# Performance work log

Measured on AMD Instinct MI355X. Metric: run time of the kernel, lower is better.

The kernel has to match this reference:

```python
import jax, jax.numpy as jnp
import numpy as np

NUM_CLS = 80
TOPK = 100
CONF_THRESH = 0.05
NMS_THRESH = 0.5
NKS_ALPHA = 0.6
INPUT_SIZE = (512, 512)  # (H, W)
STRIDES = (4, 8, 16, 32)
BATCH = 8


def _make_pixel_location():
    H, W = INPUT_SIZE
    locs = []
    for s in STRIDES:
        hs, ws = H // s, W // s
        ys, xs = np.meshgrid(np.arange(hs), np.arange(ws), indexing='ij')
        x = xs * s + s / 2.0
        y = ys * s + s / 2.0
        locs.append(np.stack([x, y, x, y], -1).reshape(-1, 4))
    return np.concatenate(locs, 0).astype(np.float32)  # [HW, 4]


def setup_inputs() -> dict:
    key = jax.random.key(0)
    pix = jnp.asarray(_make_pixel_location())
    HW = pix.shape[0]
    pred_head = jax.random.normal(key, (BATCH, HW, NUM_CLS + 5), dtype=jnp.float32)
    return {"pred_head": pred_head, "pixel_location": pix}


def _nms_single(boxes, scores, cls, valid):
    """Greedy per-class NMS on fixed-size TOPK candidates. Returns keep mask in original order."""
    N = scores.shape[0]
    order = jnp.argsort(-jnp.where(valid, scores, -jnp.inf))
    b = boxes[order]
    v = valid[order]
    c = cls[order]
    x1, y1, x2, y2 = b[:, 0], b[:, 1], b[:, 2], b[:, 3]
    areas = (x2 - x1) * (y2 - y1)
    xx1 = jnp.maximum(x1[:, None], x1[None, :])
    yy1 = jnp.maximum(y1[:, None], y1[None, :])
    xx2 = jnp.minimum(x2[:, None], x2[None, :])
    yy2 = jnp.minimum(y2[:, None], y2[None, :])
    w = jnp.maximum(1e-28, xx2 - xx1)
    h = jnp.maximum(1e-28, yy2 - yy1)
    inter = w * h
    ovr = inter / (areas[:, None] + areas[None, :] - inter)
    # original NMS is per-class: cross-class pairs never suppress
    ovr = jnp.where(c[:, None] == c[None, :], ovr, 0.0)
    idx = jnp.arange(N)

    def body(i, state):
        keep, sup = state
        ki = v[i] & jnp.logical_not(sup[i])
        keep = keep.at[i].set(ki)
        sup = sup | (ki & (ovr[i] > NMS_THRESH) & (idx > i))
        return (keep, sup)

    keep_sorted, _ = jax.lax.fori_loop(0, N, body, (jnp.zeros(N, bool), jnp.zeros(N, bool)))
    return jnp.zeros(N, bool).at[order].set(keep_sorted)


def reference(pred_head, pixel_location):
    B, HW, _ = pred_head.shape
    cls_pred = jax.nn.sigmoid(pred_head[:, :, :NUM_CLS])               # [B, HW, C]
    loc_w = jnp.array([[-1.0, -1.0, 1.0, 1.0]], dtype=pred_head.dtype)
    loc_pred = jax.nn.relu(pred_head[:, :, NUM_CLS:-1]) * loc_w + pixel_location[None]  # [B, HW, 4]
    nks = jax.nn.sigmoid(pred_head[:, :, -1:])
    nks = 1.0 / (1.0 + jnp.exp(-2.0 * nks + 1.0))
    cls_pred = jnp.power(cls_pred, (2.0 - nks) * NKS_ALPHA + 1e-14)

    def pool3x3(x):
        # torch F.max_pool2d on 3D [B,HW,C] pools 3x3 over the (HW, C) plane
        return jax.lax.reduce_window(x, -jnp.inf, jax.lax.max, (1, 3, 3), (1, 1, 1), 'SAME')

    def step(cmap, i):
        # original re-suppresses the shared heatmap on every batch iteration
        hmax = pool3x3(cmap)
        cmap = cmap * (hmax == cmap).astype(cmap.dtype)
        flat = jnp.transpose(cmap[i], (1, 0)).reshape(-1)  # class-major [C*HW], matches permute(1,0).view(-1)
        s, ind = jax.lax.top_k(flat, TOPK)
        return cmap, (s, ind)

    _, (topk_scores, topk_inds) = jax.lax.scan(step, cls_pred, jnp.arange(B))  # [B, TOPK]
    topk_cls = (topk_inds // HW).astype(jnp.int32)
    topk_hw = topk_inds % HW
    boxes = jnp.take_along_axis(loc_pred, topk_hw[:, :, None], axis=1)  # [B, TOPK, 4]
    valid = topk_scores > CONF_THRESH
    keep = jax.vmap(_nms_single)(boxes, topk_scores, topk_cls, valid)   # [B, TOPK] bool
    scale = jnp.array([INPUT_SIZE[1], INPUT_SIZE[0], INPUT_SIZE[1], INPUT_SIZE[0]], dtype=boxes.dtype)
    bboxes = jnp.clip(boxes / scale, 0.0, 1.0)
    return bboxes, topk_scores, topk_cls, keep
```

## Files before the change

### kernel.cpp

```cpp
#include <hip/hip_runtime.h>
#include <math.h>

#define BATCH   8
#define HW      21760
#define NCLS    80
#define NCH     85
#define TOPK    100
#define ABUF    128
#define CBUF    512
#define XTH     2.40f
#define STH     0x3F700000u
#define LTH     (-0.09315f)
#define RPB     128
#define TILES   170
#define F4PB    2720
#define SLOTP   128
#define NSLOT   (TILES * SLOTP)
#define NF4S    (NSLOT / 4)
#define SORTN   256
#define FBIN    256
#define FSH     12

#define LOG2E 1.44269504088896340736f
__device__ __forceinline__ float xsig(float x) { return 1.0f / (1.0f + expf(-x)); }
__device__ __forceinline__ float exact_score(const float* __restrict__ row, int c) {
    float p  = xsig(row[c]);
    float s1 = xsig(row[NCH - 1]);
    float n2 = 1.0f / (1.0f + expf(1.0f - 2.0f * s1));
    float e  = (2.0f - n2) * 0.6f + 1e-14f;
    return powf(p, e);
}
__device__ __forceinline__ float alog(float x, float en) {
    return en * __builtin_amdgcn_logf(1.0f + __builtin_amdgcn_exp2f(-LOG2E * x));
}
__device__ __forceinline__ float apxeneg(float x) {
    float s1 = __builtin_amdgcn_rcpf(1.0f + __builtin_amdgcn_exp2f(-LOG2E * x));
    float n2 = __builtin_amdgcn_rcpf(1.0f + __builtin_amdgcn_exp2f(-LOG2E * (2.0f * s1 - 1.0f)));
    return -((2.0f - n2) * 0.6f + 1e-14f);
}

__global__ __launch_bounds__(256, 4) void k1_screen(const float* __restrict__ pred,
                                                    float* __restrict__ sval, int* __restrict__ sidx,
                                                    unsigned int* __restrict__ cnt_g) {
    int blk = blockIdx.x;
    int b = blk / TILES, tile = blk - b * TILES;
    int hw0 = tile * RPB;
    int tid = threadIdx.x, lane = tid & 63;
    __shared__ float eneg[RPB + 2];
    __shared__ int   scand[CBUF];
    __shared__ int   aidx[ABUF];
    __shared__ unsigned int scn, acnt;

    float hx = 0.0f;
    if (tid < 2) {
        int hwg = (tid == 0) ? hw0 - 1 : hw0 + RPB;
        hwg = hwg < 0 ? 0 : (hwg > HW - 1 ? HW - 1 : hwg);
        hx = pred[((size_t)b * HW + hwg) * NCH + (NCH - 1)];
    }

    const float4* base4 = (const float4*)(pred + ((size_t)b * HW + hw0) * NCH);
    float4 r[11];
    #pragma unroll
    for (int j = 0; j < 10; ++j) r[j] = base4[tid + j * 256];
    bool t10 = tid < (F4PB - 2560);
    r[10] = base4[t10 ? tid + 2560 : tid];

    if (tid == 0) { scn = 0; acnt = 0; }
    if (tid < 2) eneg[tid == 0 ? 0 : RPB + 1] = apxeneg(hx);
    __syncthreads();

    #pragma unroll
    for (int j = 0; j < 11; ++j) {
        bool active = (j < 10) | t10;
        int v = (j < 10) ? tid + j * 256 : (t10 ? tid + 2560 : tid);
        int f0 = v * 4;
        int m = f0 % 85;
        float4 rj = r[j];
        if (active && m >= 81) {
            int q = 84 - m;
            float x = q == 0 ? rj.x : (q == 1 ? rj.y : (q == 2 ? rj.z : rj.w));
            int i = (f0 - m) / 85;
            eneg[i + 1] = apxeneg(x);
        }
        if (active) {
            #pragma unroll
            for (int q = 0; q < 4; ++q) {
                float x = q == 0 ? rj.x : (q == 1 ? rj.y : (q == 2 ? rj.z : rj.w));
                if (x >= XTH) {
                    int f = f0 + q;
                    int i0 = f / 85, ch = f - i0 * 85;
                    if (ch < NCLS) {
                        unsigned int pos = atomicAdd(&scn, 1u);
                        if (pos < CBUF) scand[pos] = ((i0 + 1) << 7) | ch;
                    }
                }
            }
        }
    }
    __syncthreads();
    unsigned int sn = scn < CBUF ? scn : CBUF;

    for (unsigned int k = tid; k < sn; k += 256) {
        int pk = scand[k];
        int i = pk >> 7, c = pk & 127;
        int cm = c > 0 ? c - 1 : 0, cp = c < NCLS - 1 ? c + 1 : NCLS - 1;
        int h0 = hw0 + i - 2; h0 = h0 < 0 ? 0 : h0;
        int h1 = hw0 + i - 1;
        int h2 = hw0 + i; h2 = h2 > HW - 1 ? HW - 1 : h2;
        const float* r0 = pred + (size_t)(b * HW + h0) * NCH;
        const float* r1 = pred + (size_t)(b * HW + h1) * NCH;
        const float* r2 = pred + (size_t)(b * HW + h2) * NCH;
        float x00 = r0[cm], x01 = r0[c], x02 = r0[cp];
        float x10 = r1[cm], x11 = r1[c], x12 = r1[cp];
        float x20 = r2[cm], x21 = r2[c], x22 = r2[cp];
        float e0 = eneg[i - 1], e1 = eneg[i], e2 = eneg[i + 1];
        float l00 = alog(x00, e0), l01 = alog(x01, e0), l02 = alog(x02, e0);
        float l10 = alog(x10, e1), l11 = alog(x11, e1), l12 = alog(x12, e1);
        float l20 = alog(x20, e2), l21 = alog(x21, e2), l22 = alog(x22, e2);
        float mx = fmaxf(fmaxf(fmaxf(fmaxf(l00, l01), fmaxf(l02, l10)),
                               fmaxf(fmaxf(l11, l12), fmaxf(l20, l21))), l22);
        float lv = l11;
        bool adm = (lv >= mx) && (lv >= LTH);
        unsigned long long mb = __ballot(adm);
        if (mb) {
            int ldr = __ffsll(mb) - 1;
            unsigned int base = 0;
            if (lane == ldr) base = atomicAdd(&acnt, (unsigned int)__popcll(mb));
            base = (unsigned int)__shfl((int)base, ldr);
            if (adm) {
                unsigned int pos = base + (unsigned int)__popcll(mb & ((1ULL << lane) - 1ULL));
                int gi = c * HW + hw0 + i - 1;
                if (pos < ABUF) aidx[pos] = gi;
            }
        }
    }
    __syncthreads();

    unsigned int nb = acnt < ABUF ? acnt : ABUF;
    if (tid < (int)nb) {
        int gi = aidx[tid];
        int c = gi / HW, hw = gi - c * HW;
        float ve = exact_score(pred + ((size_t)b * HW + hw) * NCH, c);
        size_t sb = ((size_t)(b * TILES + tile)) * SLOTP + tid;
        sval[sb] = ve;
        sidx[sb] = gi;
    }
    if (tid == 0) cnt_g[b * TILES + tile] = nb;
}

#define KFT 512
struct K2 { unsigned int hi, lo; };

__global__ __launch_bounds__(KFT) void k_final(const float* __restrict__ pred, const float* __restrict__ pix,
                                               const float* __restrict__ sval, const int* __restrict__ sidx,
                                               const unsigned int* __restrict__ cnt_g,
                                               float* __restrict__ out) {
    int b = blockIdx.x;
    int tid = threadIdx.x;

    __shared__ unsigned int scnt[TILES];
    __shared__ unsigned int sfx[FBIN];
    __shared__ unsigned int sedge, m;
    __shared__ unsigned long long kv[SORTN];
    __shared__ float tv[TOPK];
    __shared__ int   ti[TOPK];
    __shared__ float x1s[TOPK], y1s[TOPK], x2s[TOPK], y2s[TOPK], ar[TOPK];
    __shared__ int cls[TOPK];
    __shared__ unsigned int ovb[TOPK][4];
    __shared__ unsigned int valm[4], keepm[4];

    for (int t = tid; t < TILES; t += KFT) scnt[t] = cnt_g[b * TILES + t];
    if (tid < FBIN) sfx[tid] = 0;
    if (tid < SORTN) kv[tid] = 0ULL;
    for (int t = tid; t < TOPK * 4; t += KFT) ovb[t >> 2][t & 3] = 0;
    if (tid < 4) { valm[tid] = 0; keepm[tid] = 0; }
    if (tid == 0) { sedge = 0; m = 0; }

    const float4* sv4 = (const float4*)(sval + (size_t)b * NSLOT);
    float4 rv[11];
    #pragma unroll
    for (int j = 0; j < 11; ++j) {
        int v = j * KFT + tid;
        rv[j] = sv4[v < NF4S ? v : 0];
    }
    __syncthreads();

    #pragma unroll
    for (int j = 0; j < 11; ++j) {
        int v = j * KFT + tid;
        if (v < NF4S) {
            int t0 = v * 4;
            int blk = t0 >> 7, s0 = t0 & 127;
            int cn = (int)scnt[blk];
            #pragma unroll
            for (int q = 0; q < 4; ++q) {
                if (s0 + q < cn) {
                    float x = q == 0 ? rv[j].x : (q == 1 ? rv[j].y : (q == 2 ? rv[j].z : rv[j].w));
                    unsigned int bits = __float_as_uint(x);
                    unsigned int rel = bits >= STH ? bits - STH : 0u;
                    unsigned int bin = rel >> FSH; if (bin > FBIN - 1) bin = FBIN - 1;
                    atomicAdd(&sfx[bin], 1u);
                }
            }
        }
    }
    __syncthreads();

    if (tid < 64) {
        int lane = tid;
        unsigned int h0 = sfx[lane * 4 + 0], h1 = sfx[lane * 4 + 1];
        unsigned int h2 = sfx[lane * 4 + 2], h3 = sfx[lane * 4 + 3];
        unsigned int s3 = h3, s2 = h2 + s3, s1 = h1 + s2, s0 = h0 + s1;
        unsigned int t = s0;
        unsigned int acc = t;
        #pragma unroll
        for (int d = 1; d < 64; d <<= 1) {
            unsigned int x = (unsigned int)__shfl_down((int)acc, d);
            if (lane + d < 64) acc += x;
        }
        unsigned int above = acc - t;
        unsigned int best = 0;
        if (s0 + above >= TOPK) best = lane * 4 + 0;
        if (s1 + above >= TOPK) best = lane * 4 + 1;
        if (s2 + above >= TOPK) best = lane * 4 + 2;
        if (s3 + above >= TOPK) best = lane * 4 + 3;
        #pragma unroll
        for (int d = 32; d > 0; d >>= 1) {
            unsigned int x = (unsigned int)__shfl_xor((int)best, d);
            best = x > best ? x : best;
        }
        if (lane == 0) sedge = STH + (best << FSH);
    }
    __syncthreads();
    unsigned int edge = sedge;

    const int* si = sidx + (size_t)b * NSLOT;
    #pragma unroll
    for (int j = 0; j < 11; ++j) {
        int v = j * KFT + tid;
        if (v < NF4S) {
            int t0 = v * 4;
            int blk = t0 >> 7, s0 = t0 & 127;
            int cn = (int)scnt[blk];
            #pragma unroll
            for (int q = 0; q < 4; ++q) {
                if (s0 + q < cn) {
                    float x = q == 0 ? rv[j].x : (q == 1 ? rv[j].y : (q == 2 ? rv[j].z : rv[j].w));
                    unsigned int bits = __float_as_uint(x);
                    if (bits >= edge) {
                        unsigned int p2 = atomicAdd(&m, 1u);
                        if (p2 < SORTN)
                            kv[p2] = ((unsigned long long)bits << 32) | (unsigned int)(~(unsigned int)si[t0 + q]);
                    }
                }
            }
        }
    }
    __syncthreads();

    if (tid < 64) {
        int lane = tid;
        K2 v0, v1, v2, v3;
        { unsigned long long q;
          q = kv[0 * 64 + lane]; v0.hi = (unsigned int)(q >> 32); v0.lo = (unsigned int)q;
          q = kv[1 * 64 + lane]; v1.hi = (unsigned int)(q >> 32); v1.lo = (unsigned int)q;
          q = kv[2 * 64 + lane]; v2.hi = (unsigned int)(q >> 32); v2.lo = (unsigned int)q;
          q = kv[3 * 64 + lane]; v3.hi = (unsigned int)(q >> 32); v3.lo = (unsigned int)q; }
        K2 vr[4] = {v0, v1, v2, v3};

        #pragma unroll
        for (int kk = 2; kk <= 256; kk <<= 1) {
            #pragma unroll
            for (int j = 128; j > 0; j >>= 1) {
                if (j > (kk >> 1)) continue;
                if (j >= 64) {
                    int rb = j >> 6;
                    #pragma unroll
                    for (int r = 0; r < 4; ++r) {
                        if (!(r & rb)) {
                            int il = r * 64 + lane;
                            bool amax = ((il & kk) == 0);
                            K2 &a = vr[r], &bq = vr[r | rb];
                            bool altb = (a.hi < bq.hi) || (a.hi == bq.hi && a.lo < bq.lo);
                            bool blta = (bq.hi < a.hi) || (bq.hi == a.hi && bq.lo < a.lo);
                            if (amax ? altb : blta) { K2 tt = a; a = bq; bq = tt; }
                        }
                    }
                } else {
                    #pragma unroll
                    for (int r = 0; r < 4; ++r) {
                        K2 p;
                        p.hi = (unsigned int)__shfl_xor((int)vr[r].hi, j);
                        p.lo = (unsigned int)__shfl_xor((int)vr[r].lo, j);
                        int ie = r * 64 + lane;
                        bool lower = ((ie & j) == 0);
                        bool amax = ((ie & kk) == 0) ? lower : !lower;
                        bool pltv = (p.hi < vr[r].hi) || (p.hi == vr[r].hi && p.lo < vr[r].lo);
                        K2 mx = pltv ? vr[r] : p;
                        K2 mn = pltv ? p : vr[r];
                        vr[r] = amax ? mx : mn;
                    }
                }
            }
        }
        #pragma unroll
        for (int r = 0; r < 2; ++r) {
            int k = r * 64 + lane;
            if (k < TOPK) {
                bool z = (vr[r].hi == 0u) && (vr[r].lo == 0u);
                tv[k] = z ? 0.0f : __uint_as_float(vr[r].hi);
                ti[k] = z ? 0 : (int)(~vr[r].lo);
            }
        }
    }
    __syncthreads();

    if (tid < TOPK) {
        int k = tid;
        int idx = ti[k];
        int c = idx / HW, hw = idx - c * HW;
        const float* p = pred + ((size_t)(b * HW + hw)) * NCH + NCLS;
        float a0 = fmaxf(p[0], 0.0f), a1 = fmaxf(p[1], 0.0f);
        float a2 = fmaxf(p[2], 0.0f), a3 = fmaxf(p[3], 0.0f);
        float px = pix[hw * 4 + 0], py = pix[hw * 4 + 1];
        float X1 = px - a0, Y1 = py - a1, X2 = px + a2, Y2 = py + a3;
        x1s[k] = X1; y1s[k] = Y1; x2s[k] = X2; y2s[k] = Y2;
        ar[k] = (X2 - X1) * (Y2 - Y1);
        cls[k] = c;
        if (tv[k] > 0.05f) atomicOr(&valm[k >> 5], 1u << (k & 31));
    }
    __syncthreads();

    for (int t = tid; t < TOPK * TOPK; t += KFT) {
        int i = t / TOPK, j = t - i * TOPK;
        if (j > i && cls[i] == cls[j]) {
            float xx1 = fmaxf(x1s[i], x1s[j]), yy1 = fmaxf(y1s[i], y1s[j]);
            float xx2 = fminf(x2s[i], x2s[j]), yy2 = fminf(y2s[i], y2s[j]);
            float w = fmaxf(1e-28f, xx2 - xx1), h = fmaxf(1e-28f, yy2 - yy1);
            float inter = w * h;
            float ovr = inter / (ar[i] + ar[j] - inter);
            if (ovr > 0.5f) atomicOr(&ovb[i][j >> 5], 1u << (j & 31));
        }
    }
    __syncthreads();

    if (tid < 64) {
        int lane = tid;
        unsigned int a0 = ovb[lane][0], a1 = ovb[lane][1], a2 = ovb[lane][2], a3 = ovb[lane][3];
        unsigned int b0 = 0, b1 = 0, b2 = 0, b3 = 0;
        if (lane < TOPK - 64) { b0 = ovb[64 + lane][0]; b1 = ovb[64 + lane][1]; b2 = ovb[64 + lane][2]; b3 = ovb[64 + lane][3]; }
        unsigned int vm0 = valm[0], vm1 = valm[1], vm2 = valm[2], vm3 = valm[3];
        unsigned int sup0 = 0, sup1 = 0, sup2 = 0, sup3 = 0;
        unsigned int km0 = 0, km1 = 0, km2 = 0, km3 = 0;
        for (int i = 0; i < TOPK; ++i) {
            unsigned int r0, r1, r2, r3;
            if (i < 64) {
                r0 = (unsigned int)__shfl((int)a0, i); r1 = (unsigned int)__shfl((int)a1, i);
                r2 = (unsigned int)__shfl((int)a2, i); r3 = (unsigned int)__shfl((int)a3, i);
            } else {
                int l = i - 64;
                r0 = (unsigned int)__shfl((int)b0, l); r1 = (unsigned int)__shfl((int)b1, l);
                r2 = (unsigned int)__shfl((int)b2, l); r3 = (unsigned int)__shfl((int)b3, l);
            }
            unsigned int w = (unsigned int)(i >> 5), bit = 1u << (i & 31);
            unsigned int vmw  = w == 0 ? vm0  : (w == 1 ? vm1  : (w == 2 ? vm2  : vm3));
            unsigned int supw = w == 0 ? sup0 : (w == 1 ? sup1 : (w == 2 ? sup2 : sup3));
            bool ki = ((vmw & bit) != 0) && ((supw & bit) == 0);
            if (ki) {
                if (w == 0) km0 |= bit; else if (w == 1) km1 |= bit; else if (w == 2) km2 |= bit; else km3 |= bit;
                sup0 |= r0; sup1 |= r1; sup2 |= r2; sup3 |= r3;
            }
        }
        if (lane == 0) { keepm[0] = km0; keepm[1] = km1; keepm[2] = km2; keepm[3] = km3; }
    }
    __syncthreads();

    if (tid < TOPK) {
        int k = tid;
        const float inv = 1.0f / 512.0f;
        float b0 = fminf(fmaxf(x1s[k] * inv, 0.0f), 1.0f);
        float b1 = fminf(fmaxf(y1s[k] * inv, 0.0f), 1.0f);
        float b2 = fminf(fmaxf(x2s[k] * inv, 0.0f), 1.0f);
        float b3 = fminf(fmaxf(y2s[k] * inv, 0.0f), 1.0f);
        size_t o = (size_t)b * TOPK + k;
        out[o * 4 + 0] = b0; out[o * 4 + 1] = b1;
        out[o * 4 + 2] = b2; out[o * 4 + 3] = b3;
        out[(size_t)BATCH * TOPK * 4 + o] = tv[k];
        out[(size_t)BATCH * TOPK * 5 + o] = (float)cls[k];
        out[(size_t)BATCH * TOPK * 6 + o] = ((keepm[k >> 5] >> (k & 31)) & 1u) ? 1.0f : 0.0f;
    }
}

extern "C" void kernel_launch(void* const* d_in, const int* in_sizes, int n_in,
                              void* d_out, int out_size, void* d_ws, size_t ws_size,
                              hipStream_t stream) {
    const float* pred = (const float*)d_in[0];
    const float* pix  = (const float*)d_in[1];
    float* out = (float*)d_out;

    char* ws = (char*)d_ws;
    size_t off = 0;
    unsigned int* cnt_g = (unsigned int*)(ws + off); off += (size_t)BATCH * TILES * sizeof(unsigned int);
    off = (off + 255) & ~(size_t)255;
    float* sval = (float*)(ws + off);                off += (size_t)BATCH * NSLOT * sizeof(float);
    int*   sidx = (int*)(ws + off);                  off += (size_t)BATCH * NSLOT * sizeof(int);


    k1_screen<<<BATCH * TILES, 256, 0, stream>>>(pred, sval, sidx, cnt_g);
    k_final  <<<BATCH,         KFT, 0, stream>>>(pred, pix, sval, sidx, cnt_g, out);
}
```

Before: 136.9 us.

## Add middle kernel to build partial histograms and compact candidate lists

Adds a k_mid kernel with 80 blocks (10 groups per batch). Each block builds a partial score histogram and compacts the valid slot candidates into a dense list. k_final now sums the partial histograms and scans only the compacted lists, instead of one 512-thread block per batch reading all 21760 slots. The aim is to spread the histogram and filtering work across more CUs, at the cost of an extra kernel launch and another round trip through global memory.

```diff
diff --git a/kernel.cpp b/kernel.cpp
--- a/kernel.cpp
+++ b/kernel.cpp
@@ -16,7 +16,11 @@
 #define F4PB    2720
 #define SLOTP   128
 #define NSLOT   (TILES * SLOTP)
-#define NF4S    (NSLOT / 4)
+#define GROUPS  10
+#define TPG     17
+#define GSLOT   (TPG * SLOTP)
+#define GF4     (GSLOT / 4)
+#define CCAP    GSLOT
 #define SORTN   256
 #define FBIN    256
 #define FSH     12
@@ -148,18 +152,65 @@
     if (tid == 0) cnt_g[b * TILES + tile] = nb;
 }
 
+__global__ __launch_bounds__(256) void k_mid(const float* __restrict__ sval, const int* __restrict__ sidx,
+                                             const unsigned int* __restrict__ cnt_g,
+                                             unsigned int* __restrict__ hist_part,
+                                             unsigned int* __restrict__ clist,
+                                             unsigned int* __restrict__ ccnt) {
+    int blk = blockIdx.x;
+    int b = blk / GROUPS, g = blk - b * GROUPS;
+    int tid = threadIdx.x;
+    __shared__ unsigned int hist[FBIN];
+    __shared__ unsigned int tcnt[TPG];
+    __shared__ unsigned int cc;
+    if (tid < FBIN) hist[tid] = 0;
+    if (tid < TPG) tcnt[tid] = cnt_g[b * TILES + g * TPG + tid];
+    if (tid == 0) cc = 0;
+    size_t sbase = ((size_t)(b * TILES + g * TPG)) * SLOTP;
+    const float4* sv4 = (const float4*)(sval + sbase);
+    const int4*   si4 = (const int4*)(sidx + sbase);
+    unsigned int* cl = clist + (size_t)blk * CCAP * 2;
+    __syncthreads();
+
+    for (int v = tid; v < GF4; v += 256) {
+        float4 x4 = sv4[v];
+        int4   i4 = si4[v];
+        int t0 = v * 4;
+        int tile = t0 >> 7, s0 = t0 & 127;
+        int cn = (int)tcnt[tile];
+        #pragma unroll
+        for (int q = 0; q < 4; ++q) {
+            if (s0 + q < cn) {
+                float x = q == 0 ? x4.x : (q == 1 ? x4.y : (q == 2 ? x4.z : x4.w));
+                int  ix = q == 0 ? i4.x : (q == 1 ? i4.y : (q == 2 ? i4.z : i4.w));
+                unsigned int bits = __float_as_uint(x);
+                unsigned int rel = bits >= STH ? bits - STH : 0u;
+                unsigned int bin = rel >> FSH; if (bin > FBIN - 1) bin = FBIN - 1;
+                atomicAdd(&hist[bin], 1u);
+                unsigned int p = atomicAdd(&cc, 1u);
+                cl[p * 2 + 0] = bits;
+                cl[p * 2 + 1] = (unsigned int)ix;
+            }
+        }
+    }
+    __syncthreads();
+    if (tid < FBIN) hist_part[(size_t)blk * FBIN + tid] = hist[tid];
+    if (tid == 0) ccnt[blk] = cc;
+}
+
 #define KFT 512
 struct K2 { unsigned int hi, lo; };
 
 __global__ __launch_bounds__(KFT) void k_final(const float* __restrict__ pred, const float* __restrict__ pix,
-                                               const float* __restrict__ sval, const int* __restrict__ sidx,
-                                               const unsigned int* __restrict__ cnt_g,
+                                               const unsigned int* __restrict__ hist_part,
+                                               const unsigned int* __restrict__ clist,
+                                               const unsigned int* __restrict__ ccnt,
                                                float* __restrict__ out) {
     int b = blockIdx.x;
     int tid = threadIdx.x;
 
-    __shared__ unsigned int scnt[TILES];
     __shared__ unsigned int sfx[FBIN];
+    __shared__ unsigned int gcnt[GROUPS];
     __shared__ unsigned int sedge, m;
     __shared__ unsigned long long kv[SORTN];
     __shared__ float tv[TOPK];
@@ -169,40 +220,16 @@
     __shared__ unsigned int ovb[TOPK][4];
     __shared__ unsigned int valm[4], keepm[4];
 
-    for (int t = tid; t < TILES; t += KFT) scnt[t] = cnt_g[b * TILES + t];
-    if (tid < FBIN) sfx[tid] = 0;
+    if (tid < GROUPS) gcnt[tid] = ccnt[b * GROUPS + tid];
     if (tid < SORTN) kv[tid] = 0ULL;
     for (int t = tid; t < TOPK * 4; t += KFT) ovb[t >> 2][t & 3] = 0;
     if (tid < 4) { valm[tid] = 0; keepm[tid] = 0; }
     if (tid == 0) { sedge = 0; m = 0; }
-
-    const float4* sv4 = (const float4*)(sval + (size_t)b * NSLOT);
-    float4 rv[11];
-    #pragma unroll
-    for (int j = 0; j < 11; ++j) {
-        int v = j * KFT + tid;
-        rv[j] = sv4[v < NF4S ? v : 0];
-    }
-    __syncthreads();
-
-    #pragma unroll
-    for (int j = 0; j < 11; ++j) {
-        int v = j * KFT + tid;
-        if (v < NF4S) {
-            int t0 = v * 4;
-            int blk = t0 >> 7, s0 = t0 & 127;
-            int cn = (int)scnt[blk];
-            #pragma unroll
-            for (int q = 0; q < 4; ++q) {
-                if (s0 + q < cn) {
-                    float x = q == 0 ? rv[j].x : (q == 1 ? rv[j].y : (q == 2 ? rv[j].z : rv[j].w));
-                    unsigned int bits = __float_as_uint(x);
-                    unsigned int rel = bits >= STH ? bits - STH : 0u;
-                    unsigned int bin = rel >> FSH; if (bin > FBIN - 1) bin = FBIN - 1;
-                    atomicAdd(&sfx[bin], 1u);
-                }
-            }
-        }
+    if (tid < FBIN) {
+        unsigned int h = 0;
+        for (int g = 0; g < GROUPS; ++g)
+            h += hist_part[((size_t)(b * GROUPS + g)) * FBIN + tid];
+        sfx[tid] = h;
     }
     __syncthreads();
 
@@ -234,25 +261,16 @@
     __syncthreads();
     unsigned int edge = sedge;
 
-    const int* si = sidx + (size_t)b * NSLOT;
-    #pragma unroll
-    for (int j = 0; j < 11; ++j) {
-        int v = j * KFT + tid;
-        if (v < NF4S) {
-            int t0 = v * 4;
-            int blk = t0 >> 7, s0 = t0 & 127;
-            int cn = (int)scnt[blk];
-            #pragma unroll
-            for (int q = 0; q < 4; ++q) {
-                if (s0 + q < cn) {
-                    float x = q == 0 ? rv[j].x : (q == 1 ? rv[j].y : (q == 2 ? rv[j].z : rv[j].w));
-                    unsigned int bits = __float_as_uint(x);
-                    if (bits >= edge) {
-                        unsigned int p2 = atomicAdd(&m, 1u);
-                        if (p2 < SORTN)
-                            kv[p2] = ((unsigned long long)bits << 32) | (unsigned int)(~(unsigned int)si[t0 + q]);
-                    }
-                }
+    for (int g = 0; g < GROUPS; ++g) {
+        int cn = (int)gcnt[g];
+        const unsigned int* cl = clist + (size_t)(b * GROUPS + g) * CCAP * 2;
+        for (int k = tid; k < cn; k += KFT) {
+            unsigned int bits = cl[k * 2 + 0];
+            if (bits >= edge) {
+                unsigned int idx = cl[k * 2 + 1];
+                unsigned int p2 = atomicAdd(&m, 1u);
+                if (p2 < SORTN)
+                    kv[p2] = ((unsigned long long)bits << 32) | (unsigned int)(~idx);
             }
         }
     }
@@ -404,8 +422,14 @@
     off = (off + 255) & ~(size_t)255;
     float* sval = (float*)(ws + off);                off += (size_t)BATCH * NSLOT * sizeof(float);
     int*   sidx = (int*)(ws + off);                  off += (size_t)BATCH * NSLOT * sizeof(int);
-
-
-    k1_screen<<<BATCH * TILES, 256, 0, stream>>>(pred, sval, sidx, cnt_g);
-    k_final  <<<BATCH,         KFT, 0, stream>>>(pred, pix, sval, sidx, cnt_g, out);
-}
+    off = (off + 255) & ~(size_t)255;
+    unsigned int* hist_part = (unsigned int*)(ws + off); off += (size_t)BATCH * GROUPS * FBIN * sizeof(unsigned int);
+    unsigned int* ccnt = (unsigned int*)(ws + off);      off += (size_t)BATCH * GROUPS * sizeof(unsigned int);
+    off = (off + 255) & ~(size_t)255;
+    unsigned int* clist = (unsigned int*)(ws + off); off += (size_t)BATCH * GROUPS * CCAP * 2 * sizeof(unsigned int);
+
+
+    k1_screen<<<BATCH * TILES,  256, 0, stream>>>(pred, sval, sidx, cnt_g);
+    k_mid    <<<BATCH * GROUPS, 256, 0, stream>>>(sval, sidx, cnt_g, hist_part, clist, ccnt);
+    k_final  <<<BATCH,          KFT, 0, stream>>>(pred, pix, hist_part, clist, ccnt, out);
+}
```

After: 141.0 us. 3.0% more time.
